# Kernel optimization log

Measured on AMD Instinct MI355X. Metric: run time of the kernel, lower is better.

## Reference

```python
import jax, jax.numpy as jnp
import numpy as np
import math

B, N, C, A, H = 1, 320, 128, 32, 4  # batch, n_res, rep_2d channels, attn channels, heads


def _layernorm(x, w, b, eps=1e-5):
    mu = jnp.mean(x, axis=-1, keepdims=True)
    var = jnp.var(x, axis=-1, keepdims=True)
    return (x - mu) * jax.lax.rsqrt(var + eps) * w + b


def setup_inputs() -> dict:
    key = jax.random.key(0)
    ks = jax.random.split(key, 12)
    s = 0.02
    return {
        "x2d": jax.random.normal(ks[0], (B, N, N, C), dtype=jnp.float32),
        "mask": jnp.ones((B, N, N), dtype=jnp.float32),
        "norm_w": jnp.ones((C,), dtype=jnp.float32),
        "norm_b": jnp.zeros((C,), dtype=jnp.float32),
        "Wq": jax.random.normal(ks[1], (C, A * H), dtype=jnp.float32) * s,
        "Wk": jax.random.normal(ks[2], (C, A * H), dtype=jnp.float32) * s,
        "Wv": jax.random.normal(ks[3], (C, A * H), dtype=jnp.float32) * s,
        "Wb": jax.random.normal(ks[4], (C, H), dtype=jnp.float32) * s,
        "Wg": jax.random.normal(ks[5], (C, A * H), dtype=jnp.float32) * s,
        "bg": jnp.zeros((A * H,), dtype=jnp.float32),
        "Wo": jax.random.normal(ks[6], (A * H, C), dtype=jnp.float32) * s,
        "bo": jnp.zeros((C,), dtype=jnp.float32),
    }


def reference(x2d, mask, norm_w, norm_b, Wq, Wk, Wv, Wb, Wg, bg, Wo, bo):
    xn = _layernorm(x2d, norm_w, norm_b)                      # [B,N,N,C]
    # note: torch .view(..., A, H) splits the output channel as (A, H)
    q = (xn @ Wq).reshape(B, N, N, A, H)
    k = (xn @ Wk).reshape(B, N, N, A, H)
    v = (xn @ Wv).reshape(B, N, N, A, H)
    b = xn @ Wb                                               # [B,N,N,H] -> b[b,j,k,h]
    g = jax.nn.sigmoid((xn @ Wg + bg).reshape(B, N, N, A, H))
    w = jnp.einsum('bijch,bikch->bijkh', q, k) / math.sqrt(A)
    # torch: b.unsqueeze(1).transpose(2,3) => w[b,i,j,k,h] += b[b,k,j,h]
    w = w + jnp.transpose(b, (0, 2, 1, 3))[:, None]           # [B,1,N,N,H]
    w = (w + 100.0) * mask[:, :, None, :, None] - 100.0
    w = jax.nn.softmax(w, axis=-2)                            # over k
    out = jnp.einsum('bijkh,bikch->bijch', w, v) * g          # [B,N,N,A,H]
    out = out.reshape(B, N, N, A * H) @ Wo + bo               # [B,N,N,C]
    out = out * mask[..., None]
    return out
```

## Files before the change

kernel.cpp:

```cpp
#include <hip/hip_runtime.h>
#include <hip/hip_bf16.h>
#include <math.h>

#define N 320
#define C 128
#define A 32
#define H 4
#define NPOS (N*N)

typedef __attribute__((ext_vector_type(8))) __bf16 bf16x8;
typedef __attribute__((ext_vector_type(16))) float f32x16;

union frag_u { int4 i; bf16x8 v; unsigned u[4]; };

#define MFMA32(va, vb, vc) __builtin_amdgcn_mfma_f32_32x32x16_bf16((va), (vb), (vc), 0, 0, 0)

#define WAVE_LDS_FENCE() do { \
    asm volatile("s_waitcnt lgkmcnt(0)" ::: "memory"); \
    __builtin_amdgcn_sched_barrier(0); \
} while (0)

static __device__ __forceinline__ unsigned pk_bf16(float lo, float hi) {
    union { __hip_bfloat162 h; unsigned u; } cv;
    cv.h = __float22bfloat162_rn(make_float2(lo, hi));
    return cv.u;
}

static __device__ __forceinline__ float bf16_to_f32(unsigned short u) {
    union { unsigned u; float f; } c;
    c.u = ((unsigned)u) << 16;
    return c.f;
}

__global__ __launch_bounds__(256)
void wprep_kernel(const float* __restrict__ Wq,
                  const float* __restrict__ Wk,
                  const float* __restrict__ Wv,
                  const float* __restrict__ Wg,
                  const float* __restrict__ Wo,
                  unsigned short* __restrict__ WF) {
    const float isq = 0.17677669529663687f;
    int tid = blockIdx.x * 256 + threadIdx.x;
    int lane = tid & 63;
    int kk = (tid >> 6) & 7;
    int ct = (tid >> 9) & 3;
    int mat = tid >> 11;
    const float* src = (mat == 0) ? Wq : (mat == 1) ? Wk : (mat == 2) ? Wv
                     : (mat == 3) ? Wg : Wo;
    float scl = (mat == 0) ? isq : 1.0f;
    int col = ct * 32 + (lane & 31);
    int c0 = kk * 16 + (lane >> 5) * 8;
    float v[8];
    #pragma unroll
    for (int e = 0; e < 8; e++) {
        int rr = c0 + e;
        int srow = (mat == 4) ? (((rr & 31) << 2) | (rr >> 5)) : rr;
        v[e] = src[(size_t)srow * 128 + col] * scl;
    }
    int4 out;
    out.x = pk_bf16(v[0], v[1]);
    out.y = pk_bf16(v[2], v[3]);
    out.z = pk_bf16(v[4], v[5]);
    out.w = pk_bf16(v[6], v[7]);
    *(int4*)((char*)WF + (size_t)tid * 16) = out;
}

__global__ __launch_bounds__(256)
void ln_proj_kernel(const float* __restrict__ x2d,
                    const float* __restrict__ norm_w,
                    const float* __restrict__ norm_b,
                    const float* __restrict__ Wb,
                    const float* __restrict__ bg,
                    const unsigned short* __restrict__ WF,
                    unsigned short* __restrict__ Qb,
                    unsigned short* __restrict__ Kb,
                    unsigned short* __restrict__ Vta,
                    unsigned short* __restrict__ Gb,
                    float* __restrict__ BpT) {
    __shared__ __align__(16) unsigned char xnb[64 * 256];
    __shared__ float stage[4][32 * 65];

    const int t = threadIdx.x;
    const int gpos0 = blockIdx.x * 64;

    {
        const int r = t >> 2, s = t & 3;
        const float4* src = (const float4*)(x2d + (size_t)(gpos0 + r) * 128 + s * 32);
        float4 xv[8];
        #pragma unroll
        for (int u = 0; u < 8; u++) xv[u] = src[u];
        float sum = 0.f, sq = 0.f;
        #pragma unroll
        for (int u = 0; u < 8; u++) {
            sum += xv[u].x + xv[u].y + xv[u].z + xv[u].w;
            sq += xv[u].x * xv[u].x + xv[u].y * xv[u].y
                + xv[u].z * xv[u].z + xv[u].w * xv[u].w;
        }
        sum += __shfl_xor(sum, 1); sum += __shfl_xor(sum, 2);
        sq  += __shfl_xor(sq, 1);  sq  += __shfl_xor(sq, 2);
        float mean = sum * (1.0f / 128.0f);
        float var  = sq * (1.0f / 128.0f) - mean * mean;
        float rstd = rsqrtf(var + 1e-5f);

        const float4* wsrc = (const float4*)(norm_w + s * 32);
        const float4* bsrc = (const float4*)(norm_b + s * 32);
        const float4* wb4  = (const float4*)Wb;
        float pb0 = 0.f, pb1 = 0.f, pb2 = 0.f, pb3 = 0.f;
        float4 xe;
        #pragma unroll
        for (int u = 0; u < 8; u++) {
            float4 wv = wsrc[u], bv = bsrc[u], x4 = xv[u];
            float4 xn;
            xn.x = (x4.x - mean) * rstd * wv.x + bv.x;
            xn.y = (x4.y - mean) * rstd * wv.y + bv.y;
            xn.z = (x4.z - mean) * rstd * wv.z + bv.z;
            xn.w = (x4.w - mean) * rstd * wv.w + bv.w;
            int cb = s * 32 + u * 4;
            float4 w0 = wb4[cb + 0], w1 = wb4[cb + 1], w2 = wb4[cb + 2], w3 = wb4[cb + 3];
            pb0 = fmaf(xn.x, w0.x, fmaf(xn.y, w1.x, fmaf(xn.z, w2.x, fmaf(xn.w, w3.x, pb0))));
            pb1 = fmaf(xn.x, w0.y, fmaf(xn.y, w1.y, fmaf(xn.z, w2.y, fmaf(xn.w, w3.y, pb1))));
            pb2 = fmaf(xn.x, w0.z, fmaf(xn.y, w1.z, fmaf(xn.z, w2.z, fmaf(xn.w, w3.z, pb2))));
            pb3 = fmaf(xn.x, w0.w, fmaf(xn.y, w1.w, fmaf(xn.z, w2.w, fmaf(xn.w, w3.w, pb3))));
            if (u & 1) {
                int g = s * 4 + (u >> 1);
                int4 gr;
                gr.x = pk_bf16(xe.x, xe.y);
                gr.y = pk_bf16(xe.z, xe.w);
                gr.z = pk_bf16(xn.x, xn.y);
                gr.w = pk_bf16(xn.z, xn.w);
                *(int4*)(xnb + r * 256 + ((g ^ (r & 7)) << 4)) = gr;
            } else {
                xe = xn;
            }
        }
        pb0 += __shfl_xor(pb0, 1); pb0 += __shfl_xor(pb0, 2);
        pb1 += __shfl_xor(pb1, 1); pb1 += __shfl_xor(pb1, 2);
        pb2 += __shfl_xor(pb2, 1); pb2 += __shfl_xor(pb2, 2);
        pb3 += __shfl_xor(pb3, 1); pb3 += __shfl_xor(pb3, 2);
        float pbsel = (s == 0) ? pb0 : (s == 1) ? pb1 : (s == 2) ? pb2 : pb3;
        int r1 = gpos0 / N;
        int r2 = (gpos0 % N) + r;
        BpT[(size_t)s * NPOS + (size_t)r2 * N + r1] = pbsel;
    }
    __syncthreads();

    const int lane = t & 63;
    const int w = t >> 6;
    const int col = lane & 31;
    const int hi = lane >> 5;

    frag_u af[2][8];
    #pragma unroll
    for (int rt = 0; rt < 2; rt++)
        #pragma unroll
        for (int kk = 0; kk < 8; kk++) {
            int row = rt * 32 + col;
            af[rt][kk].i = *(const int4*)(xnb + row * 256 + (((kk * 2 + hi) ^ (row & 7)) << 4));
        }

    const char* wf = (const char*)WF + (size_t)w * 4 * 8 * 1024;
    float* stage_w = stage[w];

    for (int ct = 0; ct < 4; ct++) {
        f32x16 acc0, acc1;
        #pragma unroll
        for (int r = 0; r < 16; r++) { acc0[r] = 0.f; acc1[r] = 0.f; }
        #pragma unroll
        for (int kk = 0; kk < 8; kk++) {
            frag_u bf;
            bf.i = *(const int4*)(wf + (ct * 8 + kk) * 1024 + lane * 16);
            acc0 = MFMA32(af[0][kk].v, bf.v, acc0);
            acc1 = MFMA32(af[1][kk].v, bf.v, acc1);
        }
        #pragma unroll
        for (int r = 0; r < 16; r++) {
            int patr = (r & 3) + 8 * (r >> 2) + 4 * hi;
            stage_w[col * 65 + patr] = acc0[r];
            stage_w[col * 65 + 32 + patr] = acc1[r];
        }
        WAVE_LDS_FENCE();
        if (w < 2) {
            char* dst = (w == 0) ? (char*)Qb : (char*)Kb;
            #pragma unroll
            for (int h = 0; h < 4; h++) {
                float f[8];
                #pragma unroll
                for (int u = 0; u < 8; u++) f[u] = stage_w[(u * 4 + h) * 65 + lane];
                int4 val;
                val.x = pk_bf16(f[0], f[1]);
                val.y = pk_bf16(f[2], f[3]);
                val.z = pk_bf16(f[4], f[5]);
                val.w = pk_bf16(f[6], f[7]);
                *(int4*)(dst + ((size_t)h * NPOS + gpos0 + lane) * 64 + ct * 16) = val;
            }
        } else if (w == 2) {
            int cc = lane & 31, half = lane >> 5;
            int plane = (cc & 3) * 32 + ct * 8 + (cc >> 2);
            unsigned pk[16];
            #pragma unroll
            for (int j2 = 0; j2 < 16; j2++)
                pk[j2] = pk_bf16(stage_w[cc * 65 + half * 32 + 2 * j2],
                                 stage_w[cc * 65 + half * 32 + 2 * j2 + 1]);
            int4* dst = (int4*)((char*)Vta + ((size_t)plane * NPOS + gpos0 + half * 32) * 2);
            dst[0] = make_int4(pk[0], pk[1], pk[2], pk[3]);
            dst[1] = make_int4(pk[4], pk[5], pk[6], pk[7]);
            dst[2] = make_int4(pk[8], pk[9], pk[10], pk[11]);
            dst[3] = make_int4(pk[12], pk[13], pk[14], pk[15]);
        } else {
            #pragma unroll
            for (int h = 0; h < 4; h++) {
                float f[8];
                #pragma unroll
                for (int u = 0; u < 8; u++) {
                    float z = stage_w[(u * 4 + h) * 65 + lane] + bg[ct * 32 + u * 4 + h];
                    f[u] = 1.0f / (1.0f + __expf(-z));
                }
                int4 val;
                val.x = pk_bf16(f[0], f[1]);
                val.y = pk_bf16(f[2], f[3]);
                val.z = pk_bf16(f[4], f[5]);
                val.w = pk_bf16(f[6], f[7]);
                *(int4*)((char*)Gb + ((size_t)h * NPOS + gpos0 + lane) * 64 + ct * 16) = val;
            }
        }
        WAVE_LDS_FENCE();
    }
}

__global__ __launch_bounds__(320, 2)
void attn_kernel(const unsigned short* __restrict__ Qb,
                 const unsigned short* __restrict__ Kb,
                 const unsigned short* __restrict__ Vta,
                 const unsigned short* __restrict__ Gb,
                 const float* __restrict__ BpT,
                 const float* __restrict__ mask,
                 unsigned short* __restrict__ Ob) {
    __shared__ __align__(16) unsigned char smem[40960];
    __shared__ float mparr[320];
    __shared__ float m2arr[320];
    unsigned char* Klds = smem;
    unsigned char* Vlds = smem + 20480;

    const int i = blockIdx.x >> 2;
    const int h = blockIdx.x & 3;
    const int t = threadIdx.x;
    const int lane = t & 63;
    const int w = t >> 6;
    const int col = lane & 31;
    const int hi = lane >> 5;
    const int jt0 = w * 64;

    frag_u qf[2][2];
    const char* qbase = (const char*)Qb + ((size_t)h * NPOS + (size_t)i * N) * 64;
    #pragma unroll
    for (int jt = 0; jt < 2; ++jt) {
        int jrow = jt0 + jt * 32 + col;
        #pragma unroll
        for (int cf = 0; cf < 2; ++cf)
            qf[jt][cf].i = *(const int4*)(qbase + (size_t)jrow * 64 + cf * 32 + hi * 16);
    }

    const char* kbsrc = (const char*)Kb + ((size_t)h * NPOS + (size_t)i * N) * 64;
    #pragma unroll
    for (int it = 0; it < 4; ++it) {
        int tt = t + it * 320;
        int k = tt >> 2, gc = tt & 3;
        int4 val = *(const int4*)(kbsrc + (size_t)k * 64 + gc * 16);
        *(int4*)(Klds + k * 64 + ((gc ^ ((k >> 1) & 3)) << 4)) = val;
    }
    const char* vbsrc = (const char*)Vta + ((size_t)h * 32 * NPOS + (size_t)i * N) * 2;
    #pragma unroll
    for (int it = 0; it < 4; ++it) {
        int tt = t + it * 320;
        int a = tt / 40, kg = tt % 40;
        int4 val = *(const int4*)(vbsrc + (size_t)a * NPOS * 2 + kg * 16);
        *(int4*)(Vlds + a * 640 + ((kg ^ (a & 7)) << 4)) = val;
    }
    {
        int kt_ = t >> 5, hi_ = (t >> 4) & 1, r_ = t & 15;
        int k = kt_ * 32 + (r_ & 3) + 8 * (r_ >> 2) + 4 * hi_;
        float m_ = mask[(size_t)i * N + k];
        mparr[t] = m_;
        m2arr[t] = fmaf(100.f, m_, -100.f);
    }
    __syncthreads();

    f32x16 accO[2];
    #pragma unroll
    for (int r = 0; r < 16; ++r) { accO[0][r] = 0.f; accO[1][r] = 0.f; }
    float lsum[2] = { 0.f, 0.f };

    const float* br0 = BpT + (size_t)h * NPOS + (size_t)(jt0 + col) * N + 4 * hi;
    const float* br1 = br0 + (size_t)32 * N;

    float4 b0[4], b1[4];
    #pragma unroll
    for (int q = 0; q < 4; ++q) b0[q] = *(const float4*)(br0 + 8 * q);

#define PROCESS_JT(JT, BB)                                                      \
    {                                                                           \
        f32x16 S;                                                               \
        _Pragma("unroll") for (int r = 0; r < 16; ++r) S[r] = 0.f;              \
        __builtin_amdgcn_s_setprio(1);                                          \
        S = MFMA32(kf0.v, qf[JT][0].v, S);                                      \
        S = MFMA32(kf1.v, qf[JT][1].v, S);                                      \
        __builtin_amdgcn_s_setprio(0);                                          \
        float pe[16];                                                           \
        float l0 = 0.f, l1 = 0.f, l2 = 0.f, l3 = 0.f;                           \
        _Pragma("unroll") for (int q = 0; q < 4; ++q) {                         \
            float sv0 = fmaf(S[4*q+0] + BB[q].x, mk4[q].x, m2v[q].x);           \
            float sv1 = fmaf(S[4*q+1] + BB[q].y, mk4[q].y, m2v[q].y);           \
            float sv2 = fmaf(S[4*q+2] + BB[q].z, mk4[q].z, m2v[q].z);           \
            float sv3 = fmaf(S[4*q+3] + BB[q].w, mk4[q].w, m2v[q].w);           \
            pe[4*q+0] = __expf(sv0); pe[4*q+1] = __expf(sv1);                   \
            pe[4*q+2] = __expf(sv2); pe[4*q+3] = __expf(sv3);                   \
            l0 += pe[4*q+0]; l1 += pe[4*q+1];                                   \
            l2 += pe[4*q+2]; l3 += pe[4*q+3];                                   \
        }                                                                       \
        lsum[JT] += (l0 + l1) + (l2 + l3);                                      \
        unsigned p[8];                                                          \
        _Pragma("unroll") for (int q = 0; q < 8; ++q)                           \
            p[q] = pk_bf16(pe[2 * q], pe[2 * q + 1]);                           \
        unsigned x0 = p[0], y0 = p[2];                                          \
        unsigned x1 = p[1], y1 = p[3];                                          \
        unsigned x2 = p[4], y2 = p[6];                                          \
        unsigned x3 = p[5], y3 = p[7];                                          \
        asm("v_permlane32_swap_b32 %0, %1" : "+v"(x0), "+v"(y0));               \
        asm("v_permlane32_swap_b32 %0, %1" : "+v"(x1), "+v"(y1));               \
        asm("v_permlane32_swap_b32 %0, %1" : "+v"(x2), "+v"(y2));               \
        asm("v_permlane32_swap_b32 %0, %1" : "+v"(x3), "+v"(y3));               \
        frag_u bf0, bf1;                                                        \
        bf0.u[0] = x0; bf0.u[1] = x1; bf0.u[2] = y0; bf0.u[3] = y1;             \
        bf1.u[0] = x2; bf1.u[1] = x3; bf1.u[2] = y2; bf1.u[3] = y3;             \
        __builtin_amdgcn_s_setprio(1);                                          \
        accO[JT] = MFMA32(vf0.v, bf0.v, accO[JT]);                              \
        accO[JT] = MFMA32(vf1.v, bf1.v, accO[JT]);                              \
        __builtin_amdgcn_s_setprio(0);                                          \
    }

    for (int kt = 0; kt < 10; ++kt) {
        const int kbase = kt * 32;
        const int krow = kbase + col;
        frag_u kf0, kf1, vf0, vf1;
        kf0.i = *(const int4*)(Klds + krow * 64 + (((0 + hi) ^ ((krow >> 1) & 3)) << 4));
        kf1.i = *(const int4*)(Klds + krow * 64 + (((2 + hi) ^ ((krow >> 1) & 3)) << 4));
        vf0.i = *(const int4*)(Vlds + col * 640 + (((kt * 4 + 0 + hi) ^ (col & 7)) << 4));
        vf1.i = *(const int4*)(Vlds + col * 640 + (((kt * 4 + 2 + hi) ^ (col & 7)) << 4));

        float4 mk4[4], m2v[4];
        const float* mp  = mparr + kbase + hi * 16;
        const float* m2p = m2arr + kbase + hi * 16;
        #pragma unroll
        for (int q = 0; q < 4; ++q) {
            mk4[q] = *(const float4*)(mp + 4 * q);
            m2v[q] = *(const float4*)(m2p + 4 * q);
        }

        #pragma unroll
        for (int q = 0; q < 4; ++q) b1[q] = *(const float4*)(br1 + kbase + 8 * q);

        PROCESS_JT(0, b0)

        if (kt < 9) {
            #pragma unroll
            for (int q = 0; q < 4; ++q) b0[q] = *(const float4*)(br0 + kbase + 32 + 8 * q);
        }

        PROCESS_JT(1, b1)
    }
#undef PROCESS_JT

    __syncthreads();
    float* st = (float*)(smem + w * 8192);

    #pragma unroll
    for (int jt = 0; jt < 2; ++jt) {
        float lt = lsum[jt] + __shfl_xor(lsum[jt], 32);
        float inv = 1.0f / lt;
        #pragma unroll
        for (int r = 0; r < 16; ++r) {
            const int a = (r & 3) + 8 * (r >> 2) + 4 * hi;
            st[col * 33 + a] = accO[jt][r] * inv;
        }
        WAVE_LDS_FENCE();
        {
            int jj = lane & 31;
            int ah0 = hi * 16;
            int jrow = jt0 + jt * 32 + jj;
            const char* gsrc = (const char*)Gb + (((size_t)h * NPOS + (size_t)i * N + jrow) * 32 + ah0) * 2;
            int4 g0 = *(const int4*)gsrc;
            int4 g1 = *(const int4*)(gsrc + 16);
            unsigned gw[8] = { (unsigned)g0.x, (unsigned)g0.y, (unsigned)g0.z, (unsigned)g0.w,
                               (unsigned)g1.x, (unsigned)g1.y, (unsigned)g1.z, (unsigned)g1.w };
            unsigned pk8[8];
            #pragma unroll
            for (int e = 0; e < 8; ++e) {
                float ge0 = bf16_to_f32((unsigned short)(gw[e] & 0xffffu));
                float ge1 = bf16_to_f32((unsigned short)(gw[e] >> 16));
                pk8[e] = pk_bf16(st[jj * 33 + ah0 + 2 * e + 0] * ge0,
                                 st[jj * 33 + ah0 + 2 * e + 1] * ge1);
            }
            char* dst = (char*)Ob + (((size_t)i * N + jrow) * 128 + h * 32 + ah0) * 2;
            *(int4*)dst = make_int4(pk8[0], pk8[1], pk8[2], pk8[3]);
            *(int4*)(dst + 16) = make_int4(pk8[4], pk8[5], pk8[6], pk8[7]);
        }
        WAVE_LDS_FENCE();
    }
}

__global__ __launch_bounds__(256)
void outproj_kernel(const unsigned short* __restrict__ Ob,
                    const unsigned short* __restrict__ WoF,
                    const float* __restrict__ bo,
                    const float* __restrict__ mask,
                    float* __restrict__ out) {
    __shared__ __align__(16) unsigned char obs[64 * 256];
    __shared__ float stage[4][32 * 65];

    const int t = threadIdx.x;
    const int gpos0 = blockIdx.x * 64;

    {
        const int r = t >> 2, s = t & 3;
        const char* src = (const char*)Ob + ((size_t)(gpos0 + r) * 128 + s * 32) * 2;
        #pragma unroll
        for (int u = 0; u < 4; ++u) {
            int4 v = *(const int4*)(src + u * 16);
            int g = s * 4 + u;
            *(int4*)(obs + r * 256 + ((g ^ (r & 7)) << 4)) = v;
        }
    }
    __syncthreads();

    const int lane = t & 63;
    const int w = t >> 6;
    const int col = lane & 31;
    const int hi = lane >> 5;

    f32x16 acc0, acc1;
    float bocol = bo[w * 32 + col];
    #pragma unroll
    for (int r = 0; r < 16; ++r) { acc0[r] = bocol; acc1[r] = bocol; }

    const char* wf = (const char*)WoF + (size_t)w * 8 * 1024;
    #pragma unroll
    for (int kk = 0; kk < 8; ++kk) {
        frag_u bf, a0, a1;
        bf.i = *(const int4*)(wf + kk * 1024 + lane * 16);
        int row0 = col, row1 = 32 + col;
        a0.i = *(const int4*)(obs + row0 * 256 + (((kk * 2 + hi) ^ (row0 & 7)) << 4));
        a1.i = *(const int4*)(obs + row1 * 256 + (((kk * 2 + hi) ^ (row1 & 7)) << 4));
        acc0 = MFMA32(a0.v, bf.v, acc0);
        acc1 = MFMA32(a1.v, bf.v, acc1);
    }

    float* st = stage[w];
    #pragma unroll
    for (int r = 0; r < 16; ++r) {
        int patr = (r & 3) + 8 * (r >> 2) + 4 * hi;
        st[col * 65 + patr] = acc0[r];
        st[col * 65 + 32 + patr] = acc1[r];
    }
    WAVE_LDS_FENCE();
    {
        int row = lane;
        float mv = mask[gpos0 + row];
        float4* dst = (float4*)(out + (size_t)(gpos0 + row) * 128 + w * 32);
        #pragma unroll
        for (int u = 0; u < 8; ++u) {
            float4 o;
            o.x = st[(4 * u + 0) * 65 + row] * mv;
            o.y = st[(4 * u + 1) * 65 + row] * mv;
            o.z = st[(4 * u + 2) * 65 + row] * mv;
            o.w = st[(4 * u + 3) * 65 + row] * mv;
            dst[u] = o;
        }
    }
}

extern "C" void kernel_launch(void* const* d_in, const int* in_sizes, int n_in,
                              void* d_out, int out_size, void* d_ws, size_t ws_size,
                              hipStream_t stream) {
    const float* x2d    = (const float*)d_in[0];
    const float* mask   = (const float*)d_in[1];
    const float* norm_w = (const float*)d_in[2];
    const float* norm_b = (const float*)d_in[3];
    const float* Wq     = (const float*)d_in[4];
    const float* Wk     = (const float*)d_in[5];
    const float* Wv     = (const float*)d_in[6];
    const float* Wb     = (const float*)d_in[7];
    const float* Wg     = (const float*)d_in[8];
    const float* bg     = (const float*)d_in[9];
    const float* Wo     = (const float*)d_in[10];
    const float* bo     = (const float*)d_in[11];
    float* out = (float*)d_out;

    char* ws = (char*)d_ws;
    float* BpT = (float*)ws;                                   ws += (size_t)H * NPOS * 4;
    unsigned short* Qb  = (unsigned short*)ws;                 ws += (size_t)NPOS * C * 2;
    unsigned short* Kb  = (unsigned short*)ws;                 ws += (size_t)NPOS * C * 2;
    unsigned short* Vta = (unsigned short*)ws;                 ws += (size_t)NPOS * C * 2;
    unsigned short* Gb  = (unsigned short*)ws;                 ws += (size_t)NPOS * C * 2;
    unsigned short* Ob  = (unsigned short*)ws;                 ws += (size_t)NPOS * C * 2;
    unsigned short* WF  = (unsigned short*)ws;
    unsigned short* WoF = WF + (size_t)4 * 16384;

    wprep_kernel<<<40, 256, 0, stream>>>(Wq, Wk, Wv, Wg, Wo, WF);

    ln_proj_kernel<<<NPOS / 64, 256, 0, stream>>>(x2d, norm_w, norm_b, Wb, bg,
                                                  WF, Qb, Kb, Vta, Gb, BpT);

    attn_kernel<<<N * H, 320, 0, stream>>>(Qb, Kb, Vta, Gb, BpT, mask, Ob);

    outproj_kernel<<<NPOS / 64, 256, 0, stream>>>(Ob, WoF, bo, mask, out);
}
```

Baseline: 220.5 us.

## Split Q/K/G into 16-byte planes and transpose pair bias in separate kernel

The projection kernel now writes Q, K and G as per-(head, 8-channel group) planes of 16-byte vectors, so each store and load is contiguous across positions instead of strided by 64 bytes. The transposed pair-bias write, which was scattered, is replaced by a contiguous write followed by a new tiled LDS transpose kernel. The stage buffer now aliases the xn LDS buffer through an extra barrier to cut shared memory use. This costs an extra kernel launch and an extra pass over the bias array.

Result: faster. 201.3 us (-8.7%).

```diff
diff --git a/kernel.cpp b/kernel.cpp
--- a/kernel.cpp
+++ b/kernel.cpp
@@ -66,6 +66,32 @@
 }
 
 __global__ __launch_bounds__(256)
+void btrans_kernel(const float* __restrict__ Bp, float* __restrict__ BpT) {
+    __shared__ float tile[64][65];
+    const int b = blockIdx.x;
+    const int h = b / 25;
+    const int bk = (b % 25) / 5;
+    const int bj = b % 5;
+    const int k0 = bk * 64, j0 = bj * 64;
+    const float* src = Bp + (size_t)h * NPOS;
+    float* dst = BpT + (size_t)h * NPOS;
+    const int t = threadIdx.x;
+    #pragma unroll
+    for (int u = 0; u < 16; ++u) {
+        int idx = u * 256 + t;
+        int kk = idx >> 6, jj = idx & 63;
+        tile[kk][jj] = src[(size_t)(k0 + kk) * N + j0 + jj];
+    }
+    __syncthreads();
+    #pragma unroll
+    for (int u = 0; u < 16; ++u) {
+        int idx = u * 256 + t;
+        int jj = idx >> 6, kk = idx & 63;
+        dst[(size_t)(j0 + jj) * N + k0 + kk] = tile[kk][jj];
+    }
+}
+
+__global__ __launch_bounds__(256)
 void ln_proj_kernel(const float* __restrict__ x2d,
                     const float* __restrict__ norm_w,
                     const float* __restrict__ norm_b,
@@ -76,9 +102,9 @@
                     unsigned short* __restrict__ Kb,
                     unsigned short* __restrict__ Vta,
                     unsigned short* __restrict__ Gb,
-                    float* __restrict__ BpT) {
-    __shared__ __align__(16) unsigned char xnb[64 * 256];
-    __shared__ float stage[4][32 * 65];
+                    float* __restrict__ Bp) {
+    __shared__ __align__(16) unsigned char shbuf[33280];
+    unsigned char* xnb = shbuf;
 
     const int t = threadIdx.x;
     const int gpos0 = blockIdx.x * 64;
@@ -138,9 +164,7 @@
         pb2 += __shfl_xor(pb2, 1); pb2 += __shfl_xor(pb2, 2);
         pb3 += __shfl_xor(pb3, 1); pb3 += __shfl_xor(pb3, 2);
         float pbsel = (s == 0) ? pb0 : (s == 1) ? pb1 : (s == 2) ? pb2 : pb3;
-        int r1 = gpos0 / N;
-        int r2 = (gpos0 % N) + r;
-        BpT[(size_t)s * NPOS + (size_t)r2 * N + r1] = pbsel;
+        Bp[(size_t)s * NPOS + gpos0 + r] = pbsel;
     }
     __syncthreads();
 
@@ -157,9 +181,10 @@
             int row = rt * 32 + col;
             af[rt][kk].i = *(const int4*)(xnb + row * 256 + (((kk * 2 + hi) ^ (row & 7)) << 4));
         }
+    __syncthreads();
 
     const char* wf = (const char*)WF + (size_t)w * 4 * 8 * 1024;
-    float* stage_w = stage[w];
+    float* stage_w = (float*)shbuf + w * 2080;
 
     for (int ct = 0; ct < 4; ct++) {
         f32x16 acc0, acc1;
@@ -191,7 +216,7 @@
                 val.y = pk_bf16(f[2], f[3]);
                 val.z = pk_bf16(f[4], f[5]);
                 val.w = pk_bf16(f[6], f[7]);
-                *(int4*)(dst + ((size_t)h * NPOS + gpos0 + lane) * 64 + ct * 16) = val;
+                *(int4*)(dst + ((size_t)(h * 4 + ct) * NPOS + gpos0 + lane) * 16) = val;
             }
         } else if (w == 2) {
             int cc = lane & 31, half = lane >> 5;
@@ -220,7 +245,7 @@
                 val.y = pk_bf16(f[2], f[3]);
                 val.z = pk_bf16(f[4], f[5]);
                 val.w = pk_bf16(f[6], f[7]);
-                *(int4*)((char*)Gb + ((size_t)h * NPOS + gpos0 + lane) * 64 + ct * 16) = val;
+                *(int4*)((char*)Gb + ((size_t)(h * 4 + ct) * NPOS + gpos0 + lane) * 16) = val;
             }
         }
         WAVE_LDS_FENCE();
@@ -251,22 +276,22 @@
     const int jt0 = w * 64;
 
     frag_u qf[2][2];
-    const char* qbase = (const char*)Qb + ((size_t)h * NPOS + (size_t)i * N) * 64;
+    const char* qplane = (const char*)Qb + ((size_t)(h * 4) * NPOS + (size_t)i * N) * 16;
     #pragma unroll
     for (int jt = 0; jt < 2; ++jt) {
         int jrow = jt0 + jt * 32 + col;
         #pragma unroll
-        for (int cf = 0; cf < 2; ++cf)
-            qf[jt][cf].i = *(const int4*)(qbase + (size_t)jrow * 64 + cf * 32 + hi * 16);
-    }
-
-    const char* kbsrc = (const char*)Kb + ((size_t)h * NPOS + (size_t)i * N) * 64;
+        for (int cf = 0; cf < 2; ++cf) {
+            int g = cf * 2 + hi;
+            qf[jt][cf].i = *(const int4*)(qplane + ((size_t)g * NPOS + jrow) * 16);
+        }
+    }
+
+    const char* kplane = (const char*)Kb + ((size_t)(h * 4) * NPOS + (size_t)i * N) * 16;
     #pragma unroll
     for (int it = 0; it < 4; ++it) {
-        int tt = t + it * 320;
-        int k = tt >> 2, gc = tt & 3;
-        int4 val = *(const int4*)(kbsrc + (size_t)k * 64 + gc * 16);
-        *(int4*)(Klds + k * 64 + ((gc ^ ((k >> 1) & 3)) << 4)) = val;
+        int4 val = *(const int4*)(kplane + ((size_t)it * NPOS + t) * 16);
+        *(int4*)(Klds + t * 64 + ((it ^ ((t >> 1) & 3)) << 4)) = val;
     }
     const char* vbsrc = (const char*)Vta + ((size_t)h * 32 * NPOS + (size_t)i * N) * 2;
     #pragma unroll
@@ -372,6 +397,7 @@
 
     __syncthreads();
     float* st = (float*)(smem + w * 8192);
+    const char* gplane = (const char*)Gb + ((size_t)(h * 4) * NPOS + (size_t)i * N) * 16;
 
     #pragma unroll
     for (int jt = 0; jt < 2; ++jt) {
@@ -387,9 +413,8 @@
             int jj = lane & 31;
             int ah0 = hi * 16;
             int jrow = jt0 + jt * 32 + jj;
-            const char* gsrc = (const char*)Gb + (((size_t)h * NPOS + (size_t)i * N + jrow) * 32 + ah0) * 2;
-            int4 g0 = *(const int4*)gsrc;
-            int4 g1 = *(const int4*)(gsrc + 16);
+            int4 g0 = *(const int4*)(gplane + ((size_t)(2 * hi + 0) * NPOS + jrow) * 16);
+            int4 g1 = *(const int4*)(gplane + ((size_t)(2 * hi + 1) * NPOS + jrow) * 16);
             unsigned gw[8] = { (unsigned)g0.x, (unsigned)g0.y, (unsigned)g0.z, (unsigned)g0.w,
                                (unsigned)g1.x, (unsigned)g1.y, (unsigned)g1.z, (unsigned)g1.w };
             unsigned pk8[8];
@@ -496,6 +521,7 @@
     float* out = (float*)d_out;
 
     char* ws = (char*)d_ws;
+    float* Bp  = (float*)ws;                                   ws += (size_t)H * NPOS * 4;
     float* BpT = (float*)ws;                                   ws += (size_t)H * NPOS * 4;
     unsigned short* Qb  = (unsigned short*)ws;                 ws += (size_t)NPOS * C * 2;
     unsigned short* Kb  = (unsigned short*)ws;                 ws += (size_t)NPOS * C * 2;
@@ -508,7 +534,9 @@
     wprep_kernel<<<40, 256, 0, stream>>>(Wq, Wk, Wv, Wg, Wo, WF);
 
     ln_proj_kernel<<<NPOS / 64, 256, 0, stream>>>(x2d, norm_w, norm_b, Wb, bg,
-                                                  WF, Qb, Kb, Vta, Gb, BpT);
+                                                  WF, Qb, Kb, Vta, Gb, Bp);
+
+    btrans_kernel<<<H * 25, 256, 0, stream>>>(Bp, BpT);
 
     attn_kernel<<<N * H, 320, 0, stream>>>(Qb, Kb, Vta, Gb, BpT, mask, Ob);
 
```
